# Kernel optimization log

Hardware: AMD Instinct MI355X
Metric: run time of the kernel (lower is better)

## Reference

```python
import jax, jax.numpy as jnp
import numpy as np

# VoxelGrid constants (create_empty not shown in source; fixed to a realistic dense grid)
W, L, H = 64, 64, 64
VOXEL_SIZE = 0.05
ORIGIN = 0.0  # per-axis origin, same for all batches
ROUNDING_OFFSET = 0.5
MIN_POINTS_PER_VOXEL = 10


def setup_inputs() -> dict:
    key = jax.random.key(0)
    k1, k2 = jax.random.split(key)
    B, C, N = 4, 32, 200_000
    extent = W * VOXEL_SIZE  # 3.2
    # uniform coords slightly extending past the grid so a few points are OOB
    point_coordinates = jax.random.uniform(
        k1, (B, 3, N), jnp.float32, minval=-0.02, maxval=extent + 0.02)
    point_attributes = jax.random.normal(k2, (B, C, N), jnp.float32)
    return {"point_coordinates": point_coordinates,
            "point_attributes": point_attributes}


def reference(point_coordinates, point_attributes):
    B, C, N = point_attributes.shape
    V = W * L * H
    bounds = jnp.array([W, L, H], jnp.int32)

    # point -> integer voxel coordinates (origin = 0)
    coords = jnp.floor((point_coordinates - ORIGIN) / VOXEL_SIZE
                       + ROUNDING_OFFSET).astype(jnp.int32)      # [B,3,N]
    in_bounds = jnp.all((coords >= 0) & (coords < bounds[None, :, None]),
                        axis=1)                                   # [B,N]
    flat = coords[:, 0] * (L * H) + coords[:, 1] * H + coords[:, 2]
    # route OOB points to segment V which is dropped by segment ops
    flat = jnp.where(in_bounds, flat, V)                          # [B,N]

    def per_batch(idx, attrs, mask):
        # idx [N] int32, attrs [C,N], mask [N] bool
        counts = jax.ops.segment_sum(mask.astype(jnp.int32), idx,
                                     num_segments=V)              # [V]
        vals = jnp.where(mask[None, :], attrs, -jnp.inf)          # [C,N]
        pooled = jax.ops.segment_max(vals.T, idx, num_segments=V).T  # [C,V]
        pooled = jnp.where(counts[None, :] > 0, pooled, jnp.zeros_like(pooled))
        occ = (counts >= MIN_POINTS_PER_VOXEL).astype(attrs.dtype)   # [V]
        return pooled, occ

    data, occ = jax.vmap(per_batch)(flat, point_attributes, in_bounds)
    voxeldata = data.reshape(B, C, W, L, H)
    voxeloccupancy = occ.reshape(B, 1, W, L, H)
    return voxeldata, voxeloccupancy
```

## Files before the change

kernel.cpp:

```cpp
#include <hip/hip_runtime.h>
#include <math.h>


#define GW 64
#define GL 64
#define GH 64
#define GV (GW * GL * GH)
#define NB 4
#define MIN_PTS 10

__device__ __forceinline__ int bin_coord(float x) {
    float m = __fmul_rn(x, 20.0f);
    float r = __fadd_rn(m, 0.5f);
    return (int)floorf(r);
}

__global__ void zero_kernel(uint4* __restrict__ p, int n4) {
    int i = blockIdx.x * blockDim.x + threadIdx.x;
    if (i < n4) p[i] = make_uint4(0u, 0u, 0u, 0u);
}

__global__ void hist_kernel(const float* __restrict__ coords,
                            int* __restrict__ counts,
                            int* __restrict__ vox,
                            int* __restrict__ rank,
                            int N) {
    int n = blockIdx.x * blockDim.x + threadIdx.x;
    int b = blockIdx.y;
    if (n >= N) return;
    const float* pc = coords + (size_t)b * 3 * N;
    int ix = bin_coord(pc[n]);
    int iy = bin_coord(pc[n + N]);
    int iz = bin_coord(pc[n + 2 * N]);
    bool ok = (unsigned)ix < (unsigned)GW && (unsigned)iy < (unsigned)GL &&
              (unsigned)iz < (unsigned)GH;
    int v = ok ? ((ix << 12) | (iy << 6) | iz) : -1;
    vox[(size_t)b * N + n] = v;
    if (ok) rank[(size_t)b * N + n] = atomicAdd(&counts[b * GV + v], 1);
}

__global__ void scan_blocks_kernel(const int* __restrict__ counts,
                                   int* __restrict__ offsets,
                                   int* __restrict__ blocksums) {
    __shared__ int lds[256];
    int t = threadIdx.x;
    int base = blockIdx.x * 1024 + t * 4;
    int4 c = *(const int4*)&counts[base];
    int s0 = c.x, s1 = s0 + c.y, s2 = s1 + c.z, s3 = s2 + c.w;
    lds[t] = s3;
    __syncthreads();
    for (int d = 1; d < 256; d <<= 1) {
        int v = (t >= d) ? lds[t - d] : 0;
        __syncthreads();
        if (t >= d) lds[t] += v;
        __syncthreads();
    }
    int excl = (t > 0) ? lds[t - 1] : 0;
    int4 o;
    o.x = excl; o.y = excl + s0; o.z = excl + s1; o.w = excl + s2;
    *(int4*)&offsets[base] = o;
    if (t == 255) blocksums[blockIdx.x] = lds[255];
}

__global__ void scan_sums_kernel(int* __restrict__ blocksums) {
    __shared__ int lds[256];
    int t = threadIdx.x;
    int4 c = *(const int4*)&blocksums[t * 4];
    int s0 = c.x, s1 = s0 + c.y, s2 = s1 + c.z, s3 = s2 + c.w;
    lds[t] = s3;
    __syncthreads();
    for (int d = 1; d < 256; d <<= 1) {
        int v = (t >= d) ? lds[t - d] : 0;
        __syncthreads();
        if (t >= d) lds[t] += v;
        __syncthreads();
    }
    int excl = (t > 0) ? lds[t - 1] : 0;
    int4 o;
    o.x = excl; o.y = excl + s0; o.z = excl + s1; o.w = excl + s2;
    *(int4*)&blocksums[t * 4] = o;
}

__global__ void scan_add_kernel(int* __restrict__ offsets,
                                const int* __restrict__ blocksums) {
    int i = blockIdx.x * blockDim.x + threadIdx.x;
    int s = blocksums[(i * 4) >> 10];
    int4 o = *(int4*)&offsets[i * 4];
    o.x += s; o.y += s; o.z += s; o.w += s;
    *(int4*)&offsets[i * 4] = o;
}

__global__ void sortscatter2_kernel(const float* __restrict__ attrs,
                                    const int* __restrict__ vox,
                                    const int* __restrict__ rank,
                                    const int* __restrict__ offsets,
                                    float* __restrict__ sortedT,
                                    size_t sortedStride,
                                    int b0, int N) {
    __shared__ float lds[4][64 * 33];
    __shared__ int posb[4][64];
    int t = threadIdx.x;
    int w = t >> 6;
    int l = t & 63;
    int n = blockIdx.x * 256 + t;
    int b = b0 + blockIdx.y;

    int pos = -1;
    if (n < N) {
        int v = vox[(size_t)b * N + n];
        if (v >= 0) {
            int base = offsets[b * GV];
            pos = offsets[b * GV + v] + rank[(size_t)b * N + n] - base;
        }
    }
    posb[w][l] = pos;

    if (n < N) {
        const float* pa = attrs + (size_t)b * 32 * N + n;
        float* row = &lds[w][l * 33];
#pragma unroll
        for (int c = 0; c < 32; ++c)
            row[c] = pa[(size_t)c * N];
    }
    __syncthreads();

    float* dbase = sortedT + (size_t)blockIdx.y * sortedStride;
    int j = l & 7;
#pragma unroll
    for (int s = 0; s < 8; ++s) {
        int q = s * 8 + (l >> 3);
        int p = posb[w][q];
        if (p >= 0) {
            const float* src = &lds[w][q * 33 + j * 4];
            float4 val = make_float4(src[0], src[1], src[2], src[3]);
            *(float4*)&dbase[(size_t)p * 32 + j * 4] = val;
        }
    }
}

__global__ void segmax2_kernel(const float* __restrict__ sortedT,
                               const int* __restrict__ counts,
                               const int* __restrict__ offsets,
                               float* __restrict__ vdata,
                               float* __restrict__ occ,
                               size_t sortedStride,
                               int b0) {
    __shared__ float acc[64 * 33];
    __shared__ int cntv[64];
    int t = threadIdx.x;
    int w = t >> 6;
    int lane = t & 63;
    int g = lane >> 5;
    int c = lane & 31;
    int b = b0 + blockIdx.y;
    int v0 = blockIdx.x * 64;
    int batchbase = offsets[b * GV];
    const float* sbase = sortedT + (size_t)blockIdx.y * sortedStride;

#pragma unroll
    for (int pp = 0; pp < 8; ++pp) {
        int vl = w * 16 + pp * 2 + g;
        int bv = b * GV + v0 + vl;
        int cnt = counts[bv];
        int off = offsets[bv] - batchbase;
        const float* src = sbase + (size_t)off * 32 + c;
        float m = -INFINITY;
        for (int k = 0; k < cnt; ++k)
            m = fmaxf(m, src[(size_t)k * 32]);
        acc[vl * 33 + c] = (cnt > 0) ? m : 0.0f;
        if (c == 0) cntv[vl] = cnt;
    }
    __syncthreads();

    int vv = v0 + lane;
#pragma unroll
    for (int cc = 0; cc < 8; ++cc) {
        int ch = cc * 4 + w;
        vdata[(((size_t)(b * 32 + ch)) << 18) + vv] = acc[lane * 33 + ch];
    }
    if (t < 64)
        occ[b * GV + v0 + t] = (cntv[t] >= MIN_PTS) ? 1.0f : 0.0f;
}

__global__ void scatter_idx_kernel(const int* __restrict__ vox,
                                   const int* __restrict__ rank,
                                   const int* __restrict__ offsets,
                                   int* __restrict__ sorted_idx,
                                   int N) {
    int n = blockIdx.x * blockDim.x + threadIdx.x;
    int b = blockIdx.y;
    if (n >= N) return;
    int v = vox[(size_t)b * N + n];
    if (v < 0) return;
    sorted_idx[offsets[b * GV + v] + rank[(size_t)b * N + n]] = n;
}

__global__ void segmax_kernel(const float* __restrict__ attrs,
                              const int* __restrict__ counts,
                              const int* __restrict__ offsets,
                              const int* __restrict__ sorted_idx,
                              float* __restrict__ vdata,
                              float* __restrict__ occ,
                              int N) {
    int t = blockIdx.x * blockDim.x + threadIdx.x;
    int v = t & (GV - 1);
    int c = (t >> 18) & 31;
    int b = t >> 23;
    int bv = (b << 18) | v;
    int cnt = counts[bv];
    int off = offsets[bv];
    const float* row = attrs + ((size_t)(b * 32 + c)) * N;
    float m = -INFINITY;
    for (int k = 0; k < cnt; ++k) {
        m = fmaxf(m, row[sorted_idx[off + k]]);
    }
    vdata[((size_t)(b * 32 + c) << 18) | v] = (cnt > 0) ? m : 0.0f;
    if (c == 0) occ[bv] = (cnt >= MIN_PTS) ? 1.0f : 0.0f;
}

__device__ __forceinline__ unsigned enc_f32(float f) {
    unsigned u = __float_as_uint(f);
    return (u & 0x80000000u) ? ~u : (u | 0x80000000u);
}
__device__ __forceinline__ float dec_f32(unsigned u) {
    return (u & 0x80000000u) ? __uint_as_float(u & 0x7FFFFFFFu)
                             : __uint_as_float(~u);
}

__global__ void init_kernel(uint4* __restrict__ data4, uint4* __restrict__ cnt4,
                            int nData4, int nCnt4) {
    int i = blockIdx.x * blockDim.x + threadIdx.x;
    uint4 z = make_uint4(0u, 0u, 0u, 0u);
    if (i < nData4) data4[i] = z;
    else if (i < nData4 + nCnt4) cnt4[i - nData4] = z;
}

__global__ void scatter_kernel(const float* __restrict__ coords,
                               const float* __restrict__ attrs,
                               unsigned* __restrict__ bits,
                               int* __restrict__ counts,
                               int N, int C) {
    int n = blockIdx.x * blockDim.x + threadIdx.x;
    int b = blockIdx.y;
    if (n >= N) return;
    const float* pc = coords + (size_t)b * 3 * N;
    int ix = bin_coord(pc[n]);
    int iy = bin_coord(pc[n + N]);
    int iz = bin_coord(pc[n + 2 * N]);
    if ((unsigned)ix >= (unsigned)GW || (unsigned)iy >= (unsigned)GL ||
        (unsigned)iz >= (unsigned)GH)
        return;
    int v = (ix << 12) | (iy << 6) | iz;
    atomicAdd(&counts[b * GV + v], 1);
    const float* pa = attrs + (size_t)b * C * N + n;
    unsigned* pb = bits + (size_t)b * C * GV + v;
    for (int c = 0; c < C; ++c)
        atomicMax(&pb[(size_t)c * GV], enc_f32(pa[(size_t)c * N]));
}

__global__ void finalize_kernel(unsigned* __restrict__ data,
                                const int* __restrict__ counts,
                                float* __restrict__ occ, int C) {
    int i = blockIdx.x * blockDim.x + threadIdx.x;
    int nData4 = NB * C * GV / 4;
    int nOcc4 = NB * GV / 4;
    if (i < nData4) {
        int idx = i << 2;
        int v = idx & (GV - 1);
        int b = idx / (C * GV);
        int4 cv = *(const int4*)&counts[b * GV + v];
        uint4 u = *(const uint4*)&data[idx];
        float4 r;
        r.x = cv.x > 0 ? dec_f32(u.x) : 0.0f;
        r.y = cv.y > 0 ? dec_f32(u.y) : 0.0f;
        r.z = cv.z > 0 ? dec_f32(u.z) : 0.0f;
        r.w = cv.w > 0 ? dec_f32(u.w) : 0.0f;
        *(float4*)&data[idx] = r;
    } else if (i < nData4 + nOcc4) {
        int j = (i - nData4) << 2;
        int4 cv = *(const int4*)&counts[j];
        float4 r;
        r.x = cv.x >= MIN_PTS ? 1.0f : 0.0f;
        r.y = cv.y >= MIN_PTS ? 1.0f : 0.0f;
        r.z = cv.z >= MIN_PTS ? 1.0f : 0.0f;
        r.w = cv.w >= MIN_PTS ? 1.0f : 0.0f;
        *(float4*)&occ[j] = r;
    }
}

extern "C" void kernel_launch(void* const* d_in, const int* in_sizes, int n_in,
                              void* d_out, int out_size, void* d_ws, size_t ws_size,
                              hipStream_t stream) {
    const float* coords = (const float*)d_in[0];
    const float* attrs  = (const float*)d_in[1];
    int N = in_sizes[0] / (NB * 3);
    int C = in_sizes[1] / (NB * N);

    size_t wsCommon = (size_t)(2 * NB * GV + 4096 + 2 * NB * N) * 4;
    size_t oneT  = (size_t)N * 32 * 4;
    size_t fullT = (size_t)NB * N * 32 * 4;
    size_t wsV1  = wsCommon + (size_t)NB * N * 4;

    if (C == 32 && ws_size >= wsCommon + oneT) {
        int* counts    = (int*)d_ws;
        int* offsets   = counts + (size_t)NB * GV;
        int* blocksums = offsets + (size_t)NB * GV;
        int* vox       = blocksums + 4096;
        int* rank      = vox + (size_t)NB * N;
        float* sortedT = (float*)(rank + (size_t)NB * N);
        float* vdata   = (float*)d_out;
        float* occ     = (float*)d_out + (size_t)NB * 32 * GV;

        int nCnt4 = NB * GV / 4;
        zero_kernel<<<(nCnt4 + 255) / 256, 256, 0, stream>>>((uint4*)counts,
                                                             nCnt4);
        dim3 pgrid((N + 255) / 256, NB);
        hist_kernel<<<pgrid, 256, 0, stream>>>(coords, counts, vox, rank, N);

        scan_blocks_kernel<<<NB * GV / 1024, 256, 0, stream>>>(counts, offsets,
                                                               blocksums);
        scan_sums_kernel<<<1, 256, 0, stream>>>(blocksums);
        scan_add_kernel<<<NB * GV / 1024, 256, 0, stream>>>(offsets, blocksums);

        if (ws_size >= wsCommon + fullT) {
            sortscatter2_kernel<<<dim3((N + 255) / 256, NB), 256, 0, stream>>>(
                attrs, vox, rank, offsets, sortedT, (size_t)N * 32, 0, N);
            segmax2_kernel<<<dim3(GV / 64, NB), 256, 0, stream>>>(
                sortedT, counts, offsets, vdata, occ, (size_t)N * 32, 0);
        } else {
            for (int b = 0; b < NB; ++b) {
                sortscatter2_kernel<<<dim3((N + 255) / 256, 1), 256, 0, stream>>>(
                    attrs, vox, rank, offsets, sortedT, 0, b, N);
                segmax2_kernel<<<dim3(GV / 64, 1), 256, 0, stream>>>(
                    sortedT, counts, offsets, vdata, occ, 0, b);
            }
        }
    } else if (C == 32 && ws_size >= wsV1) {
        int* counts     = (int*)d_ws;
        int* offsets    = counts + (size_t)NB * GV;
        int* blocksums  = offsets + (size_t)NB * GV;
        int* vox        = blocksums + 4096;
        int* rank       = vox + (size_t)NB * N;
        int* sorted_idx = rank + (size_t)NB * N;
        float* vdata    = (float*)d_out;
        float* occ      = (float*)d_out + (size_t)NB * 32 * GV;

        int nCnt4 = NB * GV / 4;
        zero_kernel<<<(nCnt4 + 255) / 256, 256, 0, stream>>>((uint4*)counts,
                                                             nCnt4);
        dim3 pgrid((N + 255) / 256, NB);
        hist_kernel<<<pgrid, 256, 0, stream>>>(coords, counts, vox, rank, N);

        scan_blocks_kernel<<<NB * GV / 1024, 256, 0, stream>>>(counts, offsets,
                                                               blocksums);
        scan_sums_kernel<<<1, 256, 0, stream>>>(blocksums);
        scan_add_kernel<<<NB * GV / 1024, 256, 0, stream>>>(offsets, blocksums);

        scatter_idx_kernel<<<pgrid, 256, 0, stream>>>(vox, rank, offsets,
                                                      sorted_idx, N);

        int segThreads = NB * 32 * GV;
        segmax_kernel<<<segThreads / 256, 256, 0, stream>>>(
            attrs, counts, offsets, sorted_idx, vdata, occ, N);
    } else {
        unsigned* bits = (unsigned*)d_out;
        float* occ = (float*)d_out + (size_t)NB * C * GV;
        int* counts = (int*)d_ws;
        int nData4 = NB * C * GV / 4;
        int nCnt4 = NB * GV / 4;
        int initTotal = nData4 + nCnt4;
        init_kernel<<<(initTotal + 255) / 256, 256, 0, stream>>>(
            (uint4*)d_out, (uint4*)d_ws, nData4, nCnt4);
        dim3 sgrid((N + 255) / 256, NB);
        scatter_kernel<<<sgrid, 256, 0, stream>>>(coords, attrs, bits, counts,
                                                  N, C);
        finalize_kernel<<<(initTotal + 255) / 256, 256, 0, stream>>>(
            bits, counts, occ, C);
    }
}
```

Baseline: 335.7 us.

## Fuse attribute transpose into histogram and gather via sorted indices in segmax

Replaces the post-scan scatter of full attribute rows into voxel-sorted order with a point-order transpose fused into the histogram kernel, so the attributes are read while binning happens and written coalesced. A small index-only scatter then builds sorted point indices, and the new segmax kernel gathers 128-byte attribute rows through those indices. This moves the sorted-order traffic from 32-float rows to single ints, at the cost of an extra indirection and random-row gathers in segmax. It also needs slightly more workspace for the index array.

```diff
diff --git a/kernel.cpp b/kernel.cpp
--- a/kernel.cpp
+++ b/kernel.cpp
@@ -18,6 +18,55 @@
 __global__ void zero_kernel(uint4* __restrict__ p, int n4) {
     int i = blockIdx.x * blockDim.x + threadIdx.x;
     if (i < n4) p[i] = make_uint4(0u, 0u, 0u, 0u);
+}
+
+__global__ void hist_transpose_kernel(const float* __restrict__ coords,
+                                      const float* __restrict__ attrs,
+                                      int* __restrict__ counts,
+                                      int* __restrict__ vox,
+                                      int* __restrict__ rank,
+                                      float* __restrict__ attrsT,
+                                      size_t strideT,
+                                      int b0, int N) {
+    __shared__ float lds[4][64 * 33];
+    int t = threadIdx.x;
+    int w = t >> 6;
+    int l = t & 63;
+    int n = blockIdx.x * 256 + t;
+    int b = b0 + blockIdx.y;
+
+    if (n < N) {
+        const float* pc = coords + (size_t)b * 3 * N;
+        int ix = bin_coord(pc[n]);
+        int iy = bin_coord(pc[n + N]);
+        int iz = bin_coord(pc[n + 2 * N]);
+        bool ok = (unsigned)ix < (unsigned)GW && (unsigned)iy < (unsigned)GL &&
+                  (unsigned)iz < (unsigned)GH;
+        int v = ok ? ((ix << 12) | (iy << 6) | iz) : -1;
+        vox[(size_t)b * N + n] = v;
+        if (ok) rank[(size_t)b * N + n] = atomicAdd(&counts[b * GV + v], 1);
+
+        const float* pa = attrs + (size_t)b * 32 * N + n;
+        float* row = &lds[w][l * 33];
+#pragma unroll
+        for (int c = 0; c < 32; ++c)
+            row[c] = pa[(size_t)c * N];
+    }
+    __syncthreads();
+
+    float* dbase = attrsT + (size_t)blockIdx.y * strideT;
+    int wbase = blockIdx.x * 256 + w * 64;
+    int j = l & 7;
+#pragma unroll
+    for (int s = 0; s < 8; ++s) {
+        int q = s * 8 + (l >> 3);
+        int p = wbase + q;
+        if (p < N) {
+            const float* src = &lds[w][q * 33 + j * 4];
+            float4 val = make_float4(src[0], src[1], src[2], src[3]);
+            *(float4*)&dbase[(size_t)p * 32 + j * 4] = val;
+        }
+    }
 }
 
 __global__ void hist_kernel(const float* __restrict__ coords,
@@ -39,6 +88,38 @@
     if (ok) rank[(size_t)b * N + n] = atomicAdd(&counts[b * GV + v], 1);
 }
 
+__global__ void transpose_kernel(const float* __restrict__ attrs,
+                                 float* __restrict__ attrsT,
+                                 size_t strideT, int b0, int N) {
+    __shared__ float lds[4][64 * 33];
+    int t = threadIdx.x;
+    int w = t >> 6;
+    int l = t & 63;
+    int n = blockIdx.x * 256 + t;
+    int b = b0 + blockIdx.y;
+    if (n < N) {
+        const float* pa = attrs + (size_t)b * 32 * N + n;
+        float* row = &lds[w][l * 33];
+#pragma unroll
+        for (int c = 0; c < 32; ++c)
+            row[c] = pa[(size_t)c * N];
+    }
+    __syncthreads();
+    float* dbase = attrsT + (size_t)blockIdx.y * strideT;
+    int wbase = blockIdx.x * 256 + w * 64;
+    int j = l & 7;
+#pragma unroll
+    for (int s = 0; s < 8; ++s) {
+        int q = s * 8 + (l >> 3);
+        int p = wbase + q;
+        if (p < N) {
+            const float* src = &lds[w][q * 33 + j * 4];
+            float4 val = make_float4(src[0], src[1], src[2], src[3]);
+            *(float4*)&dbase[(size_t)p * 32 + j * 4] = val;
+        }
+    }
+}
+
 __global__ void scan_blocks_kernel(const int* __restrict__ counts,
                                    int* __restrict__ offsets,
                                    int* __restrict__ blocksums) {
@@ -88,98 +169,6 @@
     int4 o = *(int4*)&offsets[i * 4];
     o.x += s; o.y += s; o.z += s; o.w += s;
     *(int4*)&offsets[i * 4] = o;
-}
-
-__global__ void sortscatter2_kernel(const float* __restrict__ attrs,
-                                    const int* __restrict__ vox,
-                                    const int* __restrict__ rank,
-                                    const int* __restrict__ offsets,
-                                    float* __restrict__ sortedT,
-                                    size_t sortedStride,
-                                    int b0, int N) {
-    __shared__ float lds[4][64 * 33];
-    __shared__ int posb[4][64];
-    int t = threadIdx.x;
-    int w = t >> 6;
-    int l = t & 63;
-    int n = blockIdx.x * 256 + t;
-    int b = b0 + blockIdx.y;
-
-    int pos = -1;
-    if (n < N) {
-        int v = vox[(size_t)b * N + n];
-        if (v >= 0) {
-            int base = offsets[b * GV];
-            pos = offsets[b * GV + v] + rank[(size_t)b * N + n] - base;
-        }
-    }
-    posb[w][l] = pos;
-
-    if (n < N) {
-        const float* pa = attrs + (size_t)b * 32 * N + n;
-        float* row = &lds[w][l * 33];
-#pragma unroll
-        for (int c = 0; c < 32; ++c)
-            row[c] = pa[(size_t)c * N];
-    }
-    __syncthreads();
-
-    float* dbase = sortedT + (size_t)blockIdx.y * sortedStride;
-    int j = l & 7;
-#pragma unroll
-    for (int s = 0; s < 8; ++s) {
-        int q = s * 8 + (l >> 3);
-        int p = posb[w][q];
-        if (p >= 0) {
-            const float* src = &lds[w][q * 33 + j * 4];
-            float4 val = make_float4(src[0], src[1], src[2], src[3]);
-            *(float4*)&dbase[(size_t)p * 32 + j * 4] = val;
-        }
-    }
-}
-
-__global__ void segmax2_kernel(const float* __restrict__ sortedT,
-                               const int* __restrict__ counts,
-                               const int* __restrict__ offsets,
-                               float* __restrict__ vdata,
-                               float* __restrict__ occ,
-                               size_t sortedStride,
-                               int b0) {
-    __shared__ float acc[64 * 33];
-    __shared__ int cntv[64];
-    int t = threadIdx.x;
-    int w = t >> 6;
-    int lane = t & 63;
-    int g = lane >> 5;
-    int c = lane & 31;
-    int b = b0 + blockIdx.y;
-    int v0 = blockIdx.x * 64;
-    int batchbase = offsets[b * GV];
-    const float* sbase = sortedT + (size_t)blockIdx.y * sortedStride;
-
-#pragma unroll
-    for (int pp = 0; pp < 8; ++pp) {
-        int vl = w * 16 + pp * 2 + g;
-        int bv = b * GV + v0 + vl;
-        int cnt = counts[bv];
-        int off = offsets[bv] - batchbase;
-        const float* src = sbase + (size_t)off * 32 + c;
-        float m = -INFINITY;
-        for (int k = 0; k < cnt; ++k)
-            m = fmaxf(m, src[(size_t)k * 32]);
-        acc[vl * 33 + c] = (cnt > 0) ? m : 0.0f;
-        if (c == 0) cntv[vl] = cnt;
-    }
-    __syncthreads();
-
-    int vv = v0 + lane;
-#pragma unroll
-    for (int cc = 0; cc < 8; ++cc) {
-        int ch = cc * 4 + w;
-        vdata[(((size_t)(b * 32 + ch)) << 18) + vv] = acc[lane * 33 + ch];
-    }
-    if (t < 64)
-        occ[b * GV + v0 + t] = (cntv[t] >= MIN_PTS) ? 1.0f : 0.0f;
 }
 
 __global__ void scatter_idx_kernel(const int* __restrict__ vox,
@@ -193,6 +182,57 @@
     int v = vox[(size_t)b * N + n];
     if (v < 0) return;
     sorted_idx[offsets[b * GV + v] + rank[(size_t)b * N + n]] = n;
+}
+
+__global__ void segmax3_kernel(const float* __restrict__ attrsT,
+                               const int* __restrict__ counts,
+                               const int* __restrict__ offsets,
+                               const int* __restrict__ sorted_idx,
+                               float* __restrict__ vdata,
+                               float* __restrict__ occ,
+                               size_t strideT,
+                               int b0) {
+    __shared__ float acc[64 * 33];
+    __shared__ int cnt_l[64];
+    __shared__ int off_l[64];
+    int t = threadIdx.x;
+    int w = t >> 6;
+    int lane = t & 63;
+    int g = lane >> 5;
+    int c = lane & 31;
+    int b = b0 + blockIdx.y;
+    int v0 = blockIdx.x * 64;
+
+    if (t < 64) {
+        int bv = b * GV + v0 + t;
+        cnt_l[t] = counts[bv];
+        off_l[t] = offsets[bv];
+    }
+    __syncthreads();
+
+    const float* sbase = attrsT + (size_t)blockIdx.y * strideT;
+#pragma unroll
+    for (int pp = 0; pp < 8; ++pp) {
+        int vl = w * 16 + pp * 2 + g;
+        int cnt = cnt_l[vl];
+        int off = off_l[vl];
+        float m = -INFINITY;
+        for (int k = 0; k < cnt; ++k) {
+            int idx = sorted_idx[off + k];
+            m = fmaxf(m, sbase[(size_t)idx * 32 + c]);
+        }
+        acc[vl * 33 + c] = (cnt > 0) ? m : 0.0f;
+    }
+    __syncthreads();
+
+    int vv = v0 + lane;
+#pragma unroll
+    for (int cc = 0; cc < 8; ++cc) {
+        int ch = cc * 4 + w;
+        vdata[(((size_t)(b * 32 + ch)) << 18) + vv] = acc[lane * 33 + ch];
+    }
+    if (t < 64)
+        occ[b * GV + v0 + t] = (cnt_l[t] >= MIN_PTS) ? 1.0f : 0.0f;
 }
 
 __global__ void segmax_kernel(const float* __restrict__ attrs,
@@ -296,46 +336,57 @@
     int N = in_sizes[0] / (NB * 3);
     int C = in_sizes[1] / (NB * N);
 
-    size_t wsCommon = (size_t)(2 * NB * GV + 4096 + 2 * NB * N) * 4;
+    size_t wsCommon = (size_t)(2 * NB * GV + 4096 + 3 * NB * N) * 4;
     size_t oneT  = (size_t)N * 32 * 4;
     size_t fullT = (size_t)NB * N * 32 * 4;
-    size_t wsV1  = wsCommon + (size_t)NB * N * 4;
 
     if (C == 32 && ws_size >= wsCommon + oneT) {
-        int* counts    = (int*)d_ws;
-        int* offsets   = counts + (size_t)NB * GV;
-        int* blocksums = offsets + (size_t)NB * GV;
-        int* vox       = blocksums + 4096;
-        int* rank      = vox + (size_t)NB * N;
-        float* sortedT = (float*)(rank + (size_t)NB * N);
-        float* vdata   = (float*)d_out;
-        float* occ     = (float*)d_out + (size_t)NB * 32 * GV;
+        int* counts     = (int*)d_ws;
+        int* offsets    = counts + (size_t)NB * GV;
+        int* blocksums  = offsets + (size_t)NB * GV;
+        int* vox        = blocksums + 4096;
+        int* rank       = vox + (size_t)NB * N;
+        int* sorted_idx = rank + (size_t)NB * N;
+        float* attrsT   = (float*)(sorted_idx + (size_t)NB * N);
+        float* vdata    = (float*)d_out;
+        float* occ      = (float*)d_out + (size_t)NB * 32 * GV;
 
         int nCnt4 = NB * GV / 4;
         zero_kernel<<<(nCnt4 + 255) / 256, 256, 0, stream>>>((uint4*)counts,
                                                              nCnt4);
         dim3 pgrid((N + 255) / 256, NB);
-        hist_kernel<<<pgrid, 256, 0, stream>>>(coords, counts, vox, rank, N);
+        bool full = (ws_size >= wsCommon + fullT);
+
+        if (full) {
+            hist_transpose_kernel<<<pgrid, 256, 0, stream>>>(
+                coords, attrs, counts, vox, rank, attrsT, (size_t)N * 32, 0, N);
+        } else {
+            hist_kernel<<<pgrid, 256, 0, stream>>>(coords, counts, vox, rank,
+                                                   N);
+        }
 
         scan_blocks_kernel<<<NB * GV / 1024, 256, 0, stream>>>(counts, offsets,
                                                                blocksums);
         scan_sums_kernel<<<1, 256, 0, stream>>>(blocksums);
         scan_add_kernel<<<NB * GV / 1024, 256, 0, stream>>>(offsets, blocksums);
 
-        if (ws_size >= wsCommon + fullT) {
-            sortscatter2_kernel<<<dim3((N + 255) / 256, NB), 256, 0, stream>>>(
-                attrs, vox, rank, offsets, sortedT, (size_t)N * 32, 0, N);
-            segmax2_kernel<<<dim3(GV / 64, NB), 256, 0, stream>>>(
-                sortedT, counts, offsets, vdata, occ, (size_t)N * 32, 0);
+        scatter_idx_kernel<<<pgrid, 256, 0, stream>>>(vox, rank, offsets,
+                                                      sorted_idx, N);
+
+        if (full) {
+            segmax3_kernel<<<dim3(GV / 64, NB), 256, 0, stream>>>(
+                attrsT, counts, offsets, sorted_idx, vdata, occ,
+                (size_t)N * 32, 0);
         } else {
             for (int b = 0; b < NB; ++b) {
-                sortscatter2_kernel<<<dim3((N + 255) / 256, 1), 256, 0, stream>>>(
-                    attrs, vox, rank, offsets, sortedT, 0, b, N);
-                segmax2_kernel<<<dim3(GV / 64, 1), 256, 0, stream>>>(
-                    sortedT, counts, offsets, vdata, occ, 0, b);
+                transpose_kernel<<<dim3((N + 255) / 256, 1), 256, 0, stream>>>(
+                    attrs, attrsT, 0, b, N);
+                segmax3_kernel<<<dim3(GV / 64, 1), 256, 0, stream>>>(
+                    attrsT, counts, offsets, sorted_idx, vdata, occ, 0, b);
             }
         }
-    } else if (C == 32 && ws_size >= wsV1) {
+    } else if (C == 32 &&
+               ws_size >= (size_t)(2 * NB * GV + 4096 + 3 * NB * N) * 4) {
         int* counts     = (int*)d_ws;
         int* offsets    = counts + (size_t)NB * GV;
         int* blocksums  = offsets + (size_t)NB * GV;
```

Result: faster. 324.0 us (-3.5%).
